# Optimization experiments

Measured on AMD Instinct MI355X. Metric: run time of the kernel, lower is better.

The kernel has to match this reference:

```python
import jax, jax.numpy as jnp
import numpy as np

B, D, H, O = 4096, 1024, 8192, 1000

def _l2norm_rows(w):
    return w / jnp.maximum(jnp.linalg.norm(w, axis=1, keepdims=True), 1e-12)

def setup_inputs() -> dict:
    key = jax.random.key(0)
    k1, k2, k3 = jax.random.split(key, 3)
    x = jax.random.normal(k1, (B, D), dtype=jnp.float32)
    kohonen_weights = _l2norm_rows(jax.random.normal(k2, (H, D), dtype=jnp.float32))
    grossberg_weights = _l2norm_rows(jax.random.normal(k3, (O, H), dtype=jnp.float32))
    return {"x": x, "kohonen_weights": kohonen_weights, "grossberg_weights": grossberg_weights}

def reference(x, kohonen_weights, grossberg_weights):
    # x: [B, D] (already flat), kohonen_weights: [H, D], grossberg_weights: [O, H]
    x2 = jnp.sum(x * x, axis=1, keepdims=True)              # [B, 1]
    w2 = jnp.sum(kohonen_weights * kohonen_weights, axis=1)  # [H]
    # Euclidean cdist via the expanded quadratic form (same as torch.cdist p=2)
    sq = x2 + w2[None, :] - 2.0 * (x @ kohonen_weights.T)    # [B, H]
    distances = jnp.sqrt(jnp.maximum(sq, 0.0))
    winners = jnp.argmin(distances, axis=1)                  # [B] int
    # one_hot @ grossberg_weights.T is exactly a row gather of grossberg_weights.T
    output = jnp.take(grossberg_weights.T, winners, axis=0)  # [B, O]
    return (output, winners)
```

## Files before the change

kernel.cpp:

```cpp
#include <hip/hip_runtime.h>
#include <hip/hip_bf16.h>
#include <hip/hip_fp16.h>


#define BB 4096
#define DD 1024
#define HH 8192
#define OO 1000

#define BM 256
#define BN 128
#define BK 64
#define NTILES (HH / BN)
#define SA_TILE (BM * BK)
#define SB_TILE (BN * BK)

typedef _Float16 f16;
typedef float f32x4 __attribute__((ext_vector_type(4)));

typedef __attribute__((address_space(3))) uint32_t lds_u32_t;
typedef __attribute__((address_space(1))) uint32_t glb_u32_t;

__device__ __forceinline__ uint32_t packkey(float v, int col) {
  uint32_t u = __float_as_uint(v);
  uint32_t mask = (uint32_t)((int32_t)u >> 31) | 0x80000000u;
  u ^= mask;
  return (u & 0xFFFFFF80u) | (uint32_t)col;
}
__device__ __forceinline__ float unpackval(uint32_t k) {
  uint32_t u = k & 0xFFFFFF80u;
  uint32_t mask = (k & 0x80000000u) ? 0x80000000u : 0xFFFFFFFFu;
  return __uint_as_float(u ^ mask);
}
__device__ __forceinline__ void kmerge(uint32_t& k1, uint32_t& k2,
                                       uint32_t o1, uint32_t o2) {
  uint32_t mn = min(k1, o1);
  uint32_t alt = (k1 > o1) ? k2 : o2;
  k1 = max(k1, o1);
  k2 = max(mn, alt);
}

__global__ __launch_bounds__(256) void cvt_kernel(
    const float* __restrict__ x, const float* __restrict__ kw,
    uint8_t* __restrict__ xq, uint8_t* __restrict__ kq,
    const float* __restrict__ G, float* __restrict__ Gt) {
  const int tid = threadIdx.x;
  const int blk = blockIdx.x;
  __shared__ float tile[32][33];
  if (blk < (BB + HH) / 4) {
#pragma unroll
    for (int i = 0; i < 4; ++i) {
      int r = blk * 4 + i;
      const float* src = (r < BB) ? (x + (size_t)r * DD)
                                  : (kw + (size_t)(r - BB) * DD);
      uint8_t* dst = (r < BB) ? (xq + (size_t)r * DD)
                              : (kq + (size_t)(r - BB) * DD);
      float4 v = ((const float4*)src)[tid];
      int p = 0;
      p = __builtin_amdgcn_cvt_pk_fp8_f32(v.x, v.y, p, false);
      p = __builtin_amdgcn_cvt_pk_fp8_f32(v.z, v.w, p, true);
      int wi = tid ^ (((r >> 3) & 1) << 1);
      ((int*)dst)[wi] = p;
    }
  } else {
    if (Gt == nullptr) return;
    const int tb = blk - (BB + HH) / 4;
    const int tx = tid & 31;
    const int ty = tid >> 5;
#pragma unroll 1
    for (int j4 = 0; j4 < 4; ++j4) {
      int tile_id = tb * 4 + j4;
      int h0 = (tile_id >> 5) * 32;
      int o0 = (tile_id & 31) * 32;
      __syncthreads();
#pragma unroll
      for (int j = 0; j < 4; ++j) {
        int o = o0 + ty + j * 8;
        if (o < OO) tile[ty + j * 8][tx] = G[(size_t)o * HH + h0 + tx];
      }
      __syncthreads();
#pragma unroll
      for (int j = 0; j < 4; ++j) {
        int o = o0 + tx;
        int h = h0 + ty + j * 8;
        if (o < OO) Gt[(size_t)h * OO + o] = tile[tx][ty + j * 8];
      }
    }
  }
}

__global__ __launch_bounds__(256, 2) void gemm_top2(
    const uint8_t* __restrict__ A, const uint8_t* __restrict__ Bt,
    uint4* __restrict__ pk) {
  __shared__ __align__(16) uint8_t sA[3][SA_TILE];
  __shared__ __align__(16) uint8_t sB[3][SB_TILE];
  __shared__ uint2 mk[BM][2];

  const int tid = threadIdx.x;
  const int w = tid >> 6;
  const int L = tid & 63;

  const int bid = blockIdx.y * gridDim.x + blockIdx.x;
  const int c8 = bid & 7;
  const int tt = bid >> 3;
  const int nx = c8 * 8 + (tt & 7);
  const int my = tt >> 3;
  const int m0 = my * BM;
  const int n0 = nx * BN;

  const int wr = w >> 1;
  const int wc = w & 1;

  f32x4 acc[8][4];
#pragma unroll
  for (int i = 0; i < 8; ++i)
#pragma unroll
    for (int j = 0; j < 4; ++j) {
      acc[i][j][0] = 0.f; acc[i][j][1] = 0.f; acc[i][j][2] = 0.f; acc[i][j][3] = 0.f;
    }

  const int lm = L & 15;
  const int lq = L >> 4;

  const uint8_t* pA[4]; int dA[4];
#pragma unroll
  for (int j = 0; j < 4; ++j) {
    int c = tid + 256 * j;
    int r = c >> 2;
    int so = ((c & 3) ^ ((r >> 1) & 3)) * 16;
    pA[j] = A + (size_t)(m0 + r) * DD + so;
    dA[j] = c * 16;
  }
  const uint8_t* pB[2]; int dB[2];
#pragma unroll
  for (int j = 0; j < 2; ++j) {
    int c = tid + 256 * j;
    int r = c >> 2;
    int so = ((c & 3) ^ ((r >> 1) & 3)) * 16;
    pB[j] = Bt + (size_t)(n0 + r) * DD + so;
    dB[j] = c * 16;
  }

  auto stage = [&](int t, int p) {
#pragma unroll
    for (int j = 0; j < 4; ++j)
      __builtin_amdgcn_global_load_lds((const glb_u32_t*)(pA[j] + (size_t)t * BK),
                                       (lds_u32_t*)(&sA[p][0] + dA[j]), 16, 0, 0);
#pragma unroll
    for (int j = 0; j < 2; ++j)
      __builtin_amdgcn_global_load_lds((const glb_u32_t*)(pB[j] + (size_t)t * BK),
                                       (lds_u32_t*)(&sB[p][0] + dB[j]), 16, 0, 0);
  };

  const int t2 = (lm >> 1) & 3;
  const int s3 = (lm >> 3) & 1;
  const int raBase = (wr * 128 + lm) * BK;
  const int rbBase = (wc * 64 + lm) * BK;
  const int off0 = ((lq >> 1) ^ t2) * 16 + ((lq & 1) ^ s3) * 8;
  const int off1 = ((2 + (lq >> 1)) ^ t2) * 16 + ((lq & 1) ^ s3) * 8;

  stage(0, 0);
  stage(1, 1);

  int cur = 0;
#pragma unroll 1
  for (int kt = 0; kt < DD / BK; ++kt) {
    if (kt == DD / BK - 1)
      asm volatile("s_waitcnt vmcnt(0) lgkmcnt(0)" ::: "memory");
    else
      asm volatile("s_waitcnt vmcnt(6) lgkmcnt(0)" ::: "memory");
    __builtin_amdgcn_s_barrier();
    asm volatile("" ::: "memory");

    if (kt < DD / BK - 2) {
      int stp = cur + 2; if (stp >= 3) stp -= 3;
      stage(kt + 2, stp);
    }

    const uint8_t* bufA = &sA[cur][0];
    const uint8_t* bufB = &sB[cur][0];

    __builtin_amdgcn_s_setprio(1);
    long long af[8], bf[4];
#pragma unroll
    for (int i = 0; i < 8; ++i)
      af[i] = *(const long long*)(bufA + raBase + i * 16 * BK + off0);
#pragma unroll
    for (int j = 0; j < 4; ++j)
      bf[j] = *(const long long*)(bufB + rbBase + j * 16 * BK + off0);
#pragma unroll
    for (int i = 0; i < 8; ++i)
#pragma unroll
      for (int j = 0; j < 4; ++j)
        acc[i][j] = __builtin_amdgcn_mfma_f32_16x16x32_fp8_fp8(af[i], bf[j], acc[i][j], 0, 0, 0);
#pragma unroll
    for (int i = 0; i < 8; ++i)
      af[i] = *(const long long*)(bufA + raBase + i * 16 * BK + off1);
#pragma unroll
    for (int j = 0; j < 4; ++j)
      bf[j] = *(const long long*)(bufB + rbBase + j * 16 * BK + off1);
#pragma unroll
    for (int i = 0; i < 8; ++i)
#pragma unroll
      for (int j = 0; j < 4; ++j)
        acc[i][j] = __builtin_amdgcn_mfma_f32_16x16x32_fp8_fp8(af[i], bf[j], acc[i][j], 0, 0, 0);
    __builtin_amdgcn_s_setprio(0);

    cur = (cur == 2) ? 0 : cur + 1;
  }

  const int col0 = wc * 64 + lm;
#pragma unroll
  for (int i = 0; i < 8; ++i) {
#pragma unroll
    for (int r = 0; r < 4; ++r) {
      uint32_t k1 = 0, k2 = 0;
#pragma unroll
      for (int j = 0; j < 4; ++j) {
        uint32_t kj = packkey(acc[i][j][r], col0 + j * 16);
        if (kj > k1) { k2 = k1; k1 = kj; }
        else k2 = max(k2, kj);
      }
#pragma unroll
      for (int msk = 1; msk < 16; msk <<= 1) {
        uint32_t o1 = (uint32_t)__shfl_xor((int)k1, msk, 64);
        uint32_t o2 = (uint32_t)__shfl_xor((int)k2, msk, 64);
        kmerge(k1, k2, o1, o2);
      }
      if (lm == 0) {
        int rl = wr * 128 + i * 16 + lq * 4 + r;
        mk[rl][wc] = make_uint2(k1, k2);
      }
    }
  }
  __syncthreads();
  {
    uint2 a = mk[tid][0], b = mk[tid][1];
    pk[(size_t)(m0 + tid) * NTILES + nx] = make_uint4(a.x, a.y, b.x, b.y);
  }
}

__global__ __launch_bounds__(256) void select_kernel(
    const float* __restrict__ x, const float* __restrict__ kw,
    const uint4* __restrict__ pk,
    const float* __restrict__ Gt, const float* __restrict__ G,
    float* __restrict__ out, float* __restrict__ out_w) {
  const int b = blockIdx.x * 4 + (threadIdx.x >> 6);
  const int L = threadIdx.x & 63;

  const float4* x4 = (const float4*)(x + (size_t)b * DD);
  float4 xv[4];
#pragma unroll
  for (int j = 0; j < 4; ++j) xv[j] = x4[L + 64 * j];

  uint4 kp = pk[(size_t)b * NTILES + L];

  double x2 = 0.0;
#pragma unroll
  for (int j = 0; j < 4; ++j)
    x2 += (double)xv[j].x * xv[j].x + (double)xv[j].y * xv[j].y +
          (double)xv[j].z * xv[j].z + (double)xv[j].w * xv[j].w;
#pragma unroll
  for (int msk = 1; msk < 64; msk <<= 1) x2 += __shfl_xor(x2, msk, 64);

  uint32_t m = max(kp.x, kp.z);
#pragma unroll
  for (int msk = 1; msk < 64; msk <<= 1)
    m = max(m, (uint32_t)__shfl_xor((int)m, msk, 64));
  const uint32_t thrk = packkey(unpackval(m) - 0.35f, 0);

  unsigned long long cand[4];
  cand[0] = __ballot(kp.x >= thrk);
  cand[1] = __ballot(kp.y >= thrk);
  cand[2] = __ballot(kp.z >= thrk);
  cand[3] = __ballot(kp.w >= thrk);

  double best = 1e300;
  int bestc = 0x7fffffff;
#pragma unroll 1
  for (int pass = 0; pass < 4; ++pass) {
    unsigned long long bits = cand[pass];
    uint32_t mykey = (pass == 0) ? kp.x : (pass == 1) ? kp.y
                    : (pass == 2) ? kp.z : kp.w;
    while (bits) {
      int tt = __ffsll((long long)bits) - 1;
      bits &= bits - 1;
      uint32_t kbt = (uint32_t)__shfl((int)mykey, tt, 64);
      int col = tt * 128 + (int)(kbt & 127u);
      const float4* k4 = (const float4*)(kw + (size_t)col * DD);
      double dot = 0.0, w2 = 0.0;
#pragma unroll
      for (int j = 0; j < 4; ++j) {
        float4 wv = k4[L + 64 * j];
        dot += (double)xv[j].x * wv.x + (double)xv[j].y * wv.y +
               (double)xv[j].z * wv.z + (double)xv[j].w * wv.w;
        w2 += (double)wv.x * wv.x + (double)wv.y * wv.y +
              (double)wv.z * wv.z + (double)wv.w * wv.w;
      }
#pragma unroll
      for (int msk = 1; msk < 64; msk <<= 1) {
        dot += __shfl_xor(dot, msk, 64);
        w2 += __shfl_xor(w2, msk, 64);
      }
      double sq = x2 + w2 - 2.0 * dot;
      if (sq < best || (sq == best && col < bestc)) { best = sq; bestc = col; }
    }
  }

  if (L == 0) out_w[b] = (float)bestc;
  if (Gt != nullptr) {
    const float4* gsrc = (const float4*)(Gt + (size_t)bestc * OO);
    float4* gdst = (float4*)(out + (size_t)b * OO);
#pragma unroll
    for (int j = 0; j < 4; ++j) {
      int q = L + 64 * j;
      if (q < OO / 4) gdst[q] = gsrc[q];
    }
  } else {
#pragma unroll 1
    for (int j = 0; j < 16; ++j) {
      int o = L + 64 * j;
      if (o < OO) out[(size_t)b * OO + o] = G[(size_t)o * HH + bestc];
    }
  }
}

extern "C" void kernel_launch(void* const* d_in, const int* in_sizes, int n_in,
                              void* d_out, int out_size, void* d_ws, size_t ws_size,
                              hipStream_t stream) {
  const float* x  = (const float*)d_in[0];
  const float* kw = (const float*)d_in[1];
  const float* gw = (const float*)d_in[2];
  float* out = (float*)d_out;
  float* out_w = out + (size_t)BB * OO;

  const size_t MB = 1024 * 1024;
  char* ws = (char*)d_ws;
  uint8_t* xq = (uint8_t*)(ws);
  uint8_t* kq = (uint8_t*)(ws + 4 * MB);
  uint4*   pk = (uint4*)(ws + 12 * MB);
  float*   Gt = (float*)(ws + 16 * MB);
  const size_t need = 16 * MB + sizeof(float) * (size_t)HH * OO;
  float* GtArg = (ws_size >= need) ? Gt : nullptr;

  int cvt_blocks = (BB + HH) / 4 + (GtArg ? 2048 : 0);
  cvt_kernel<<<cvt_blocks, 256, 0, stream>>>(x, kw, xq, kq, gw, GtArg);

  dim3 g(HH / BN, BB / BM);
  gemm_top2<<<g, 256, 0, stream>>>(xq, kq, pk);

  select_kernel<<<BB / 4, 256, 0, stream>>>(x, kw, pk, GtArg, gw, out, out_w);
}
```

Before: 222.8 us.

## Switch fp8 GEMM to 32x32x64 scaled MFMA with transposed output layout

Replaces the 16x16x32 fp8 MFMA tiles with the gfx950 32x32x64 f8f6f4 scaled MFMA (unit scales), loading 128-bit fragments per lane and swapping operand order so each lane holds a row's columns. The top-2 argmin epilogue then reduces mostly in registers and needs only one cross-half shuffle, not four butterfly stages. The fp8 quantizer drops its XOR store swizzle to match the new LDS read pattern. It aims to cut MFMA issue count, LDS read instructions and epilogue shuffles, at the cost of larger accumulator vectors and possible LDS bank conflicts.

```diff
diff --git a/kernel.cpp b/kernel.cpp
--- a/kernel.cpp
+++ b/kernel.cpp
@@ -16,7 +16,10 @@
 #define SB_TILE (BN * BK)
 
 typedef _Float16 f16;
-typedef float f32x4 __attribute__((ext_vector_type(4)));
+typedef float f32x16 __attribute__((ext_vector_type(16)));
+typedef int v8i __attribute__((ext_vector_type(8)));
+typedef int v4i __attribute__((ext_vector_type(4)));
+union Frag { v8i v; v4i h[2]; };
 
 typedef __attribute__((address_space(3))) uint32_t lds_u32_t;
 typedef __attribute__((address_space(1))) uint32_t glb_u32_t;
@@ -59,8 +62,7 @@
       int p = 0;
       p = __builtin_amdgcn_cvt_pk_fp8_f32(v.x, v.y, p, false);
       p = __builtin_amdgcn_cvt_pk_fp8_f32(v.z, v.w, p, true);
-      int wi = tid ^ (((r >> 3) & 1) << 1);
-      ((int*)dst)[wi] = p;
+      ((int*)dst)[tid] = p;
     }
   } else {
     if (Gt == nullptr) return;
@@ -111,16 +113,16 @@
   const int wr = w >> 1;
   const int wc = w & 1;
 
-  f32x4 acc[8][4];
-#pragma unroll
-  for (int i = 0; i < 8; ++i)
-#pragma unroll
-    for (int j = 0; j < 4; ++j) {
-      acc[i][j][0] = 0.f; acc[i][j][1] = 0.f; acc[i][j][2] = 0.f; acc[i][j][3] = 0.f;
-    }
-
-  const int lm = L & 15;
-  const int lq = L >> 4;
+  f32x16 acc[2][4];
+#pragma unroll
+  for (int i = 0; i < 2; ++i)
+#pragma unroll
+    for (int j = 0; j < 4; ++j)
+#pragma unroll
+      for (int q = 0; q < 16; ++q) acc[i][j][q] = 0.f;
+
+  const int l31 = L & 31;
+  const int kh = L >> 5;
 
   const uint8_t* pA[4]; int dA[4];
 #pragma unroll
@@ -152,12 +154,11 @@
                                        (lds_u32_t*)(&sB[p][0] + dB[j]), 16, 0, 0);
   };
 
-  const int t2 = (lm >> 1) & 3;
-  const int s3 = (lm >> 3) & 1;
-  const int raBase = (wr * 128 + lm) * BK;
-  const int rbBase = (wc * 64 + lm) * BK;
-  const int off0 = ((lq >> 1) ^ t2) * 16 + ((lq & 1) ^ s3) * 8;
-  const int off1 = ((2 + (lq >> 1)) ^ t2) * 16 + ((lq & 1) ^ s3) * 8;
+  const int t2 = (l31 >> 1) & 3;
+  const int off_lo = ((2 * kh) ^ t2) * 16;
+  const int off_hi = ((2 * kh + 1) ^ t2) * 16;
+  const int raBase = (wr * 128 + l31) * BK;
+  const int rbBase = (wc * 64 + l31) * BK;
 
   stage(0, 0);
   stage(1, 1);
@@ -181,57 +182,49 @@
     const uint8_t* bufB = &sB[cur][0];
 
     __builtin_amdgcn_s_setprio(1);
-    long long af[8], bf[4];
-#pragma unroll
-    for (int i = 0; i < 8; ++i)
-      af[i] = *(const long long*)(bufA + raBase + i * 16 * BK + off0);
-#pragma unroll
-    for (int j = 0; j < 4; ++j)
-      bf[j] = *(const long long*)(bufB + rbBase + j * 16 * BK + off0);
-#pragma unroll
-    for (int i = 0; i < 8; ++i)
+    Frag af[4], bf[2];
+#pragma unroll
+    for (int j = 0; j < 4; ++j) {
+      const uint8_t* base = bufA + raBase + j * 32 * BK;
+      af[j].h[0] = *(const v4i*)(base + off_lo);
+      af[j].h[1] = *(const v4i*)(base + off_hi);
+    }
+#pragma unroll
+    for (int i = 0; i < 2; ++i) {
+      const uint8_t* base = bufB + rbBase + i * 32 * BK;
+      bf[i].h[0] = *(const v4i*)(base + off_lo);
+      bf[i].h[1] = *(const v4i*)(base + off_hi);
+    }
+#pragma unroll
+    for (int i = 0; i < 2; ++i)
 #pragma unroll
       for (int j = 0; j < 4; ++j)
-        acc[i][j] = __builtin_amdgcn_mfma_f32_16x16x32_fp8_fp8(af[i], bf[j], acc[i][j], 0, 0, 0);
-#pragma unroll
-    for (int i = 0; i < 8; ++i)
-      af[i] = *(const long long*)(bufA + raBase + i * 16 * BK + off1);
-#pragma unroll
-    for (int j = 0; j < 4; ++j)
-      bf[j] = *(const long long*)(bufB + rbBase + j * 16 * BK + off1);
-#pragma unroll
-    for (int i = 0; i < 8; ++i)
-#pragma unroll
-      for (int j = 0; j < 4; ++j)
-        acc[i][j] = __builtin_amdgcn_mfma_f32_16x16x32_fp8_fp8(af[i], bf[j], acc[i][j], 0, 0, 0);
+        acc[i][j] = __builtin_amdgcn_mfma_scale_f32_32x32x64_f8f6f4(
+            bf[i].v, af[j].v, acc[i][j],
+            0 , 0 ,
+            0, 0x7F7F7F7Fu , 0, 0x7F7F7F7Fu);
     __builtin_amdgcn_s_setprio(0);
 
     cur = (cur == 2) ? 0 : cur + 1;
   }
 
-  const int col0 = wc * 64 + lm;
-#pragma unroll
-  for (int i = 0; i < 8; ++i) {
-#pragma unroll
-    for (int r = 0; r < 4; ++r) {
-      uint32_t k1 = 0, k2 = 0;
-#pragma unroll
-      for (int j = 0; j < 4; ++j) {
-        uint32_t kj = packkey(acc[i][j][r], col0 + j * 16);
+#pragma unroll
+  for (int j = 0; j < 4; ++j) {
+    uint32_t k1 = 0, k2 = 0;
+#pragma unroll
+    for (int i = 0; i < 2; ++i) {
+#pragma unroll
+      for (int q = 0; q < 16; ++q) {
+        int hcol = wc * 64 + i * 32 + (q & 3) + 8 * (q >> 2) + 4 * kh;
+        uint32_t kj = packkey(acc[i][j][q], hcol);
         if (kj > k1) { k2 = k1; k1 = kj; }
         else k2 = max(k2, kj);
       }
-#pragma unroll
-      for (int msk = 1; msk < 16; msk <<= 1) {
-        uint32_t o1 = (uint32_t)__shfl_xor((int)k1, msk, 64);
-        uint32_t o2 = (uint32_t)__shfl_xor((int)k2, msk, 64);
-        kmerge(k1, k2, o1, o2);
-      }
-      if (lm == 0) {
-        int rl = wr * 128 + i * 16 + lq * 4 + r;
-        mk[rl][wc] = make_uint2(k1, k2);
-      }
-    }
+    }
+    uint32_t o1 = (uint32_t)__shfl_xor((int)k1, 32, 64);
+    uint32_t o2 = (uint32_t)__shfl_xor((int)k2, 32, 64);
+    kmerge(k1, k2, o1, o2);
+    if (kh == 0) mk[wr * 128 + j * 32 + l31][wc] = make_uint2(k1, k2);
   }
   __syncthreads();
   {
```

Result: faster. 198.9 us (-10.7%).
